# Kernel tuning notes

Hardware: AMD Instinct MI355X
Metric: run time of the kernel (lower is better)

## Reference

```python
import jax, jax.numpy as jnp
import numpy as np

DIM = 1024
HEADS = 16
HEAD_DIM = DIM // HEADS
SCALE = float(HEAD_DIM) ** -0.5


def setup_inputs() -> dict:
    key = jax.random.key(0)
    k1, k2, k3 = jax.random.split(key, 3)
    x = jax.random.normal(k1, (4, 2048, DIM), dtype=jnp.float32)
    w_qkv = jax.random.normal(k2, (DIM, 3 * DIM), dtype=jnp.float32) * (DIM ** -0.5)
    b_qkv = jnp.zeros((3 * DIM,), dtype=jnp.float32)
    w_proj = jax.random.normal(k3, (DIM, DIM), dtype=jnp.float32) * (DIM ** -0.5)
    b_proj = jnp.zeros((DIM,), dtype=jnp.float32)
    return {"x": x, "w_qkv": w_qkv, "b_qkv": b_qkv, "w_proj": w_proj, "b_proj": b_proj}


def reference(x, w_qkv, b_qkv, w_proj, b_proj):
    B, N, D = x.shape
    # QKV projection -> [B, N, 3, H, Dh] -> split
    qkv = (x @ w_qkv + b_qkv).reshape(B, N, 3, HEADS, HEAD_DIM)
    q = qkv[:, :, 0].transpose(0, 2, 1, 3)  # [B, H, N, Dh]
    k = qkv[:, :, 1].transpose(0, 2, 1, 3)
    v = qkv[:, :, 2].transpose(0, 2, 1, 3)
    att = jnp.einsum("bhnd,bhmd->bhnm", q, k) * SCALE  # [B, H, N, N]
    att = jax.nn.softmax(att, axis=-1)
    out = jnp.einsum("bhnm,bhmd->bhnd", att, v)  # [B, H, N, Dh]
    out = out.transpose(0, 2, 1, 3).reshape(B, N, D)
    return out @ w_proj + b_proj
```

## Files before the change

### kernel.cpp

```cpp
#include <hip/hip_runtime.h>


typedef __attribute__((ext_vector_type(8))) short bf8v;
typedef __attribute__((ext_vector_type(4))) short bf4v;
typedef __attribute__((ext_vector_type(4))) float f32x4;

#define DEVINL __device__ __forceinline__

DEVINL unsigned short f2bf(float x){
    unsigned int u = __float_as_uint(x);
    return (unsigned short)((u + 0x7FFFu + ((u >> 16) & 1u)) >> 16);
}
DEVINL float bf2f(unsigned short b){ return __uint_as_float(((unsigned int)b) << 16); }

union BV { bf8v v; unsigned int u[4]; };

DEVINL void gload16(const unsigned short* g, unsigned short* l){
    __builtin_amdgcn_global_load_lds(
        (const __attribute__((address_space(1))) unsigned int*)g,
        (__attribute__((address_space(3))) unsigned int*)l, 16, 0, 0);
}

__global__ __launch_bounds__(256) void split_rm(const float* __restrict__ in,
        unsigned short* __restrict__ oh, int n4){
    int i = blockIdx.x * 256 + threadIdx.x;
    if (i >= n4) return;
    float4 v = reinterpret_cast<const float4*>(in)[i];
    float vv[4] = {v.x, v.y, v.z, v.w};
    bf4v h;
#pragma unroll
    for (int j = 0; j < 4; ++j) h[j] = (short)f2bf(vv[j]);
    *reinterpret_cast<bf4v*>(oh + (size_t)i * 4) = h;
}

__global__ __launch_bounds__(256) void transpose_split(const float* __restrict__ in,
        unsigned short* __restrict__ oh,
        int K, int N){
    __shared__ float tile[32][33];
    int n0 = blockIdx.x * 32, k0 = blockIdx.y * 32;
    int c = threadIdx.x & 31, r0 = threadIdx.x >> 5;
#pragma unroll
    for (int j = 0; j < 4; ++j){
        int r = r0 + j * 8;
        tile[r][c] = in[(size_t)(k0 + r) * N + n0 + c];
    }
    __syncthreads();
#pragma unroll
    for (int j = 0; j < 4; ++j){
        int r = r0 + j * 8;
        float v = tile[c][r];
        oh[(size_t)(n0 + r) * K + k0 + c] = f2bf(v);
    }
}

template<int EPI, int NPL>
__global__ __launch_bounds__(256) void gemm3k(
    const unsigned short* __restrict__ Ah, const unsigned short* __restrict__ Al,
    const unsigned short* __restrict__ Bh,
    const float* __restrict__ bias, float* __restrict__ outf,
    unsigned short* __restrict__ Qh,
    unsigned short* __restrict__ Kh,
    unsigned short* __restrict__ Vth)
{
    __shared__ unsigned short AldsH[3][4096];
    __shared__ unsigned short AldsL[NPL == 2 ? 3 : 1][4096];
    __shared__ unsigned short Blds [3][4096];
    const int t = threadIdx.x;
    const int l = t & 63, g = l >> 4, wv = t >> 6;
    const int wr = wv >> 1, wc = wv & 1;
    const int bm = blockIdx.y * 128, bn = blockIdx.x * 128;
    const int srow = t >> 2;
    const int scol = ((t & 3) ^ ((t >> 3) & 3)) * 8;

    f32x4 acc[4][4] = {};

    auto stage = [&](int kt, int buf){
        int klocal = kt * 32;
#pragma unroll
        for (int j = 0; j < 2; ++j){
            size_t ro = (size_t)(bm + j*64 + srow) * 1024 + klocal + scol;
            gload16(Ah + ro, &AldsH[buf][j*2048 + wv*512]);
            if (NPL == 2) gload16(Al + ro, &AldsL[buf][j*2048 + wv*512]);
            gload16(Bh + (size_t)(bn + j*64 + srow) * 1024 + klocal + scol,
                    &Blds[buf][j*2048 + wv*512]);
        }
    };
    auto compute = [&](int cur){
        bf8v afh[4], bfv[4];
#pragma unroll
        for (int mf = 0; mf < 4; ++mf){
            int ar = wr*64 + mf*16 + (l & 15);
            afh[mf] = *reinterpret_cast<const bf8v*>(
                &AldsH[cur][ar*32 + (g ^ ((ar >> 1) & 3))*8]);
        }
#pragma unroll
        for (int nf = 0; nf < 4; ++nf){
            int br = wc*64 + nf*16 + (l & 15);
            bfv[nf] = *reinterpret_cast<const bf8v*>(
                &Blds[cur][br*32 + (g ^ ((br >> 1) & 3))*8]);
        }
#pragma unroll
        for (int mf = 0; mf < 4; ++mf)
#pragma unroll
            for (int nf = 0; nf < 4; ++nf)
                acc[mf][nf] = __builtin_amdgcn_mfma_f32_16x16x32_bf16(afh[mf], bfv[nf], acc[mf][nf], 0, 0, 0);
        if (NPL == 2){
            bf8v afl[4];
#pragma unroll
            for (int mf = 0; mf < 4; ++mf){
                int ar = wr*64 + mf*16 + (l & 15);
                afl[mf] = *reinterpret_cast<const bf8v*>(
                    &AldsL[NPL == 2 ? cur : 0][ar*32 + (g ^ ((ar >> 1) & 3))*8]);
            }
#pragma unroll
            for (int mf = 0; mf < 4; ++mf)
#pragma unroll
                for (int nf = 0; nf < 4; ++nf)
                    acc[mf][nf] = __builtin_amdgcn_mfma_f32_16x16x32_bf16(afl[mf], bfv[nf], acc[mf][nf], 0, 0, 0);
        }
    };

    stage(0, 0);
    stage(1, 1);
    if constexpr (NPL == 2) asm volatile("s_waitcnt vmcnt(6)" ::: "memory");
    else                    asm volatile("s_waitcnt vmcnt(4)" ::: "memory");
    __builtin_amdgcn_s_barrier();
    __builtin_amdgcn_sched_barrier(0);

    int cur = 0, nxt = 1, nx2 = 2;
#pragma unroll 1
    for (int kt = 0; kt < 32; ++kt){
        if (kt + 2 < 32) stage(kt + 2, nx2);
        compute(cur);
        if (kt + 1 < 32){
            if (kt + 2 < 32){
                if constexpr (NPL == 2) asm volatile("s_waitcnt vmcnt(6)" ::: "memory");
                else                    asm volatile("s_waitcnt vmcnt(4)" ::: "memory");
            } else {
                asm volatile("s_waitcnt vmcnt(0)" ::: "memory");
            }
            __builtin_amdgcn_s_barrier();
            __builtin_amdgcn_sched_barrier(0);
        }
        int tmp = cur; cur = nxt; nxt = nx2; nx2 = tmp;
    }
#pragma unroll
    for (int mf = 0; mf < 4; ++mf)
#pragma unroll
    for (int nf = 0; nf < 4; ++nf)
#pragma unroll
    for (int r = 0; r < 4; ++r){
        int n = bn + wc*64 + nf*16 + (l & 15);
        int m = bm + wr*64 + mf*16 + g*4 + r;
        float v = acc[mf][nf][r] + bias[n];
        if (EPI == 0){
            int sec = n >> 10;
            int nn = n & 1023, hh = nn >> 6, dh = nn & 63;
            int bb = m >> 11, tok = m & 2047;
            if (sec == 0) v *= 0.18033688011112042f;
            unsigned short hb = f2bf(v);
            if (sec == 2){
                int tok2 = (tok & ~31) | (((tok >> 2) & 3) << 3) | (tok & 3) | (((tok >> 4) & 1) << 2);
                tok2 = (tok2 & ~31) | ((tok2 & 31) ^ (((dh >> 1) & 3) << 3));
                size_t o = ((size_t)((bb*16 + hh)*64 + dh)) * 2048 + tok2;
                Vth[o] = hb;
            } else if (sec == 1){
                size_t o = ((size_t)((bb*16 + hh)*2048 + tok)) * 64 + (dh ^ ((tok & 7) << 3));
                Kh[o] = hb;
            } else {
                size_t o = ((size_t)((bb*16 + hh)*2048 + tok)) * 64 + dh;
                Qh[o] = hb;
            }
        } else {
            outf[(size_t)m * 1024 + n] = v;
        }
    }
}

__global__ __launch_bounds__(256, 4) void attn(
    const unsigned short* __restrict__ Qh,
    const unsigned short* __restrict__ Kh,
    const unsigned short* __restrict__ Vth,
    unsigned short* __restrict__ Oh, unsigned short* __restrict__ Ol)
{
    __shared__ unsigned short Klds[3][2048];
    __shared__ unsigned short Vlds[3][2048];
    const int t = threadIdx.x, l = t & 63, g = l >> 4, wv = t >> 6;
    const int bid = (int)((blockIdx.x & 7) * 128 + (blockIdx.x >> 3));
    const int qt = bid & 15, hh = (bid >> 4) & 15, bb = bid >> 8;
    const int bh = bb * 16 + hh;
    const int q0 = qt * 128 + wv * 32;

    const unsigned short* Kbh = Kh  + (size_t)bh * 131072;
    const unsigned short* Vbh = Vth + (size_t)bh * 131072;

    const int kst = (t >> 3) * 64   + (t & 7) * 8;
    const int vst = (t >> 2) * 2048 + (t & 3) * 8;

    bf8v qh_[2][2];
#pragma unroll
    for (int nf = 0; nf < 2; ++nf){
        size_t ro = ((size_t)bh * 2048 + q0 + nf*16 + (l & 15)) * 64 + g * 8;
#pragma unroll
        for (int ks = 0; ks < 2; ++ks)
            qh_[nf][ks] = *reinterpret_cast<const bf8v*>(Qh + ro + ks*32);
    }
    f32x4 ot[4][2] = {};
    float l_run[2] = {0.f, 0.f};

    auto stage = [&](int it, int buf){
        gload16(Kbh + it*2048 + kst, &Klds[buf][wv*512]);
        gload16(Vbh + it*32   + vst, &Vlds[buf][wv*512]);
    };
    auto step = [&](int cur){
        bf8v kf[2][2], vf[4];
#pragma unroll
        for (int mf = 0; mf < 2; ++mf){
            int r = (l & 15) + 16*mf;
#pragma unroll
            for (int ks = 0; ks < 2; ++ks)
                kf[mf][ks] = *reinterpret_cast<const bf8v*>(
                    &Klds[cur][r*64 + ((g*8 + ks*32) ^ ((r & 7) << 3))]);
        }
#pragma unroll
        for (int mf = 0; mf < 4; ++mf){
            int dh = (l & 15) + 16*mf;
            vf[mf] = *reinterpret_cast<const bf8v*>(
                &Vlds[cur][dh*32 + ((g*8) ^ (((dh >> 1) & 3) << 3))]);
        }
        f32x4 s[2][2] = {};
        __builtin_amdgcn_s_setprio(1);
#pragma unroll
        for (int mf = 0; mf < 2; ++mf)
#pragma unroll
        for (int nf = 0; nf < 2; ++nf)
#pragma unroll
        for (int ks = 0; ks < 2; ++ks)
            s[mf][nf] = __builtin_amdgcn_mfma_f32_16x16x32_bf16(kf[mf][ks], qh_[nf][ks], s[mf][nf], 0,0,0);
        __builtin_amdgcn_s_setprio(0);
        BV ph[2];
#pragma unroll
        for (int nf = 0; nf < 2; ++nf){
            float p[8];
#pragma unroll
            for (int mf = 0; mf < 2; ++mf)
#pragma unroll
            for (int r = 0; r < 4; ++r)
                p[mf*4 + r] = __builtin_amdgcn_exp2f(s[mf][nf][r]);
            l_run[nf] += ((p[0]+p[1]) + (p[2]+p[3])) + ((p[4]+p[5]) + (p[6]+p[7]));
#pragma unroll
            for (int i = 0; i < 4; ++i)
                asm("v_cvt_pk_bf16_f32 %0, %1, %2"
                    : "=v"(ph[nf].u[i]) : "v"(p[2*i]), "v"(p[2*i+1]));
        }
        __builtin_amdgcn_s_setprio(1);
#pragma unroll
        for (int mf = 0; mf < 4; ++mf)
#pragma unroll
        for (int nf = 0; nf < 2; ++nf)
            ot[mf][nf] = __builtin_amdgcn_mfma_f32_16x16x32_bf16(vf[mf], ph[nf].v, ot[mf][nf], 0,0,0);
        __builtin_amdgcn_s_setprio(0);
    };

    stage(0, 0);
    stage(1, 1);
    asm volatile("s_waitcnt vmcnt(2)" ::: "memory");
    __builtin_amdgcn_s_barrier();
    __builtin_amdgcn_sched_barrier(0);

    int cur = 0, nxt = 1, nx2 = 2;
#pragma unroll 1
    for (int it = 0; it < 64; ++it){
        if (it + 2 < 64) stage(it + 2, nx2);
        step(cur);
        if (it + 1 < 64){
            if (it + 2 < 64) asm volatile("s_waitcnt vmcnt(2)" ::: "memory");
            else             asm volatile("s_waitcnt vmcnt(0)" ::: "memory");
            __builtin_amdgcn_s_barrier();
            __builtin_amdgcn_sched_barrier(0);
        }
        int tmp = cur; cur = nxt; nxt = nx2; nx2 = tmp;
    }
#pragma unroll
    for (int nf = 0; nf < 2; ++nf){
        float lr = l_run[nf];
        lr += __shfl_xor(lr, 16);
        lr += __shfl_xor(lr, 32);
        float inv = 1.f / lr;
        int tok = q0 + nf*16 + (l & 15);
#pragma unroll
        for (int mf = 0; mf < 4; ++mf){
            bf4v hv, lv;
#pragma unroll
            for (int r = 0; r < 4; ++r){
                float v = ot[mf][nf][r] * inv;
                unsigned short hb = f2bf(v);
                hv[r] = (short)hb;
                lv[r] = (short)f2bf(v - bf2f(hb));
            }
            size_t o = ((size_t)(bb * 2048 + tok)) * 1024 + hh*64 + mf*16 + g*4;
            *reinterpret_cast<bf4v*>(Oh + o) = hv;
            *reinterpret_cast<bf4v*>(Ol + o) = lv;
        }
    }
}

extern "C" void kernel_launch(void* const* d_in, const int* in_sizes, int n_in,
                              void* d_out, int out_size, void* d_ws, size_t ws_size,
                              hipStream_t stream) {
    (void)in_sizes; (void)n_in; (void)out_size; (void)ws_size;
    const float* x      = (const float*)d_in[0];
    const float* w_qkv  = (const float*)d_in[1];
    const float* b_qkv  = (const float*)d_in[2];
    const float* w_proj = (const float*)d_in[3];
    const float* b_proj = (const float*)d_in[4];
    float* out = (float*)d_out;

    char* w = (char*)d_ws;
    unsigned short* XH  = (unsigned short*)(w + 0);
    unsigned short* ATL = (unsigned short*)(w + 16777216);
    unsigned short* QH  = (unsigned short*)(w + 33554432);
    unsigned short* KH  = (unsigned short*)(w + 67108864);
    unsigned short* VTH = (unsigned short*)(w + 100663296);
    unsigned short* WQH = (unsigned short*)(w + 134217728);
    unsigned short* WPH = (unsigned short*)(w + 140509184);
    unsigned short* ATH = XH;

    split_rm<<<8192, 256, 0, stream>>>(x, XH, 2097152);
    transpose_split<<<dim3(96, 32), 256, 0, stream>>>(w_qkv, WQH, 1024, 3072);
    transpose_split<<<dim3(32, 32), 256, 0, stream>>>(w_proj, WPH, 1024, 1024);
    gemm3k<0,1><<<dim3(24, 64), 256, 0, stream>>>(XH, nullptr, WQH, b_qkv, nullptr,
                                                  QH, KH, VTH);
    attn<<<1024, 256, 0, stream>>>(QH, KH, VTH, ATH, ATL);
    gemm3k<1,2><<<dim3(8, 64), 256, 0, stream>>>(ATH, ATL, WPH, b_proj, out,
                                                 nullptr, nullptr, nullptr);
}
```

Baseline: 223.3 us.

## Process two 32-key chunks per pipeline stage in attention loop

Each iteration of the attention main loop now stages and computes 64 keys (two 32-key chunks) instead of 32, halving the iteration count and the number of barriers and waitcnt sync points. The LDS K/V ring buffers double in size and launch bounds drop from 4 to 3 blocks per SM to fit the larger footprint and register use. The cost is lower occupancy and more live score registers per wave, which could offset the savings in synchronisation overhead.

```diff
diff --git a/kernel.cpp b/kernel.cpp
--- a/kernel.cpp
+++ b/kernel.cpp
@@ -177,14 +177,14 @@
     }
 }
 
-__global__ __launch_bounds__(256, 4) void attn(
+__global__ __launch_bounds__(256, 3) void attn(
     const unsigned short* __restrict__ Qh,
     const unsigned short* __restrict__ Kh,
     const unsigned short* __restrict__ Vth,
     unsigned short* __restrict__ Oh, unsigned short* __restrict__ Ol)
 {
-    __shared__ unsigned short Klds[3][2048];
-    __shared__ unsigned short Vlds[3][2048];
+    __shared__ unsigned short Klds[3][4096];
+    __shared__ unsigned short Vlds[3][4096];
     const int t = threadIdx.x, l = t & 63, g = l >> 4, wv = t >> 6;
     const int bid = (int)((blockIdx.x & 7) * 128 + (blockIdx.x >> 3));
     const int qt = bid & 15, hh = (bid >> 4) & 15, bb = bid >> 8;
@@ -209,72 +209,86 @@
     float l_run[2] = {0.f, 0.f};
 
     auto stage = [&](int it, int buf){
-        gload16(Kbh + it*2048 + kst, &Klds[buf][wv*512]);
-        gload16(Vbh + it*32   + vst, &Vlds[buf][wv*512]);
+#pragma unroll
+        for (int kc = 0; kc < 2; ++kc){
+            int it2 = it * 2 + kc;
+            gload16(Kbh + it2*2048 + kst, &Klds[buf][kc*2048 + wv*512]);
+            gload16(Vbh + it2*32   + vst, &Vlds[buf][kc*2048 + wv*512]);
+        }
     };
     auto step = [&](int cur){
-        bf8v kf[2][2], vf[4];
-#pragma unroll
-        for (int mf = 0; mf < 2; ++mf){
-            int r = (l & 15) + 16*mf;
+        f32x4 s[4][2] = {};
+#pragma unroll
+        for (int kc = 0; kc < 2; ++kc){
+            bf8v kf[2][2];
+#pragma unroll
+            for (int mt = 0; mt < 2; ++mt){
+                int r = (l & 15) + 16*mt;
+#pragma unroll
+                for (int ks = 0; ks < 2; ++ks)
+                    kf[mt][ks] = *reinterpret_cast<const bf8v*>(
+                        &Klds[cur][kc*2048 + r*64 + ((g*8 + ks*32) ^ ((r & 7) << 3))]);
+            }
+            __builtin_amdgcn_s_setprio(1);
+#pragma unroll
+            for (int mt = 0; mt < 2; ++mt)
+#pragma unroll
+            for (int nf = 0; nf < 2; ++nf)
 #pragma unroll
             for (int ks = 0; ks < 2; ++ks)
-                kf[mf][ks] = *reinterpret_cast<const bf8v*>(
-                    &Klds[cur][r*64 + ((g*8 + ks*32) ^ ((r & 7) << 3))]);
+                s[kc*2+mt][nf] = __builtin_amdgcn_mfma_f32_16x16x32_bf16(kf[mt][ks], qh_[nf][ks], s[kc*2+mt][nf], 0,0,0);
+            __builtin_amdgcn_s_setprio(0);
+        }
+        BV ph[2][2];
+#pragma unroll
+        for (int nf = 0; nf < 2; ++nf){
+            float p[16];
+#pragma unroll
+            for (int kt = 0; kt < 4; ++kt)
+#pragma unroll
+            for (int r = 0; r < 4; ++r)
+                p[kt*4 + r] = __builtin_amdgcn_exp2f(s[kt][nf][r]);
+            float s0 = ((p[0]+p[1]) + (p[2]+p[3])) + ((p[4]+p[5]) + (p[6]+p[7]));
+            float s1 = ((p[8]+p[9]) + (p[10]+p[11])) + ((p[12]+p[13]) + (p[14]+p[15]));
+            l_run[nf] += s0 + s1;
+#pragma unroll
+            for (int kc = 0; kc < 2; ++kc)
+#pragma unroll
+            for (int i = 0; i < 4; ++i)
+                asm("v_cvt_pk_bf16_f32 %0, %1, %2"
+                    : "=v"(ph[nf][kc].u[i]) : "v"(p[kc*8 + 2*i]), "v"(p[kc*8 + 2*i + 1]));
         }
 #pragma unroll
         for (int mf = 0; mf < 4; ++mf){
             int dh = (l & 15) + 16*mf;
-            vf[mf] = *reinterpret_cast<const bf8v*>(
-                &Vlds[cur][dh*32 + ((g*8) ^ (((dh >> 1) & 3) << 3))]);
-        }
-        f32x4 s[2][2] = {};
-        __builtin_amdgcn_s_setprio(1);
-#pragma unroll
-        for (int mf = 0; mf < 2; ++mf)
-#pragma unroll
-        for (int nf = 0; nf < 2; ++nf)
-#pragma unroll
-        for (int ks = 0; ks < 2; ++ks)
-            s[mf][nf] = __builtin_amdgcn_mfma_f32_16x16x32_bf16(kf[mf][ks], qh_[nf][ks], s[mf][nf], 0,0,0);
-        __builtin_amdgcn_s_setprio(0);
-        BV ph[2];
-#pragma unroll
-        for (int nf = 0; nf < 2; ++nf){
-            float p[8];
-#pragma unroll
-            for (int mf = 0; mf < 2; ++mf)
-#pragma unroll
-            for (int r = 0; r < 4; ++r)
-                p[mf*4 + r] = __builtin_amdgcn_exp2f(s[mf][nf][r]);
-            l_run[nf] += ((p[0]+p[1]) + (p[2]+p[3])) + ((p[4]+p[5]) + (p[6]+p[7]));
-#pragma unroll
-            for (int i = 0; i < 4; ++i)
-                asm("v_cvt_pk_bf16_f32 %0, %1, %2"
-                    : "=v"(ph[nf].u[i]) : "v"(p[2*i]), "v"(p[2*i+1]));
-        }
-        __builtin_amdgcn_s_setprio(1);
-#pragma unroll
-        for (int mf = 0; mf < 4; ++mf)
-#pragma unroll
-        for (int nf = 0; nf < 2; ++nf)
-            ot[mf][nf] = __builtin_amdgcn_mfma_f32_16x16x32_bf16(vf[mf], ph[nf].v, ot[mf][nf], 0,0,0);
-        __builtin_amdgcn_s_setprio(0);
+            bf8v vf[2];
+#pragma unroll
+            for (int kc = 0; kc < 2; ++kc)
+                vf[kc] = *reinterpret_cast<const bf8v*>(
+                    &Vlds[cur][kc*2048 + dh*32 + ((g*8) ^ (((dh >> 1) & 3) << 3))]);
+            __builtin_amdgcn_s_setprio(1);
+#pragma unroll
+            for (int nf = 0; nf < 2; ++nf)
+#pragma unroll
+            for (int kc = 0; kc < 2; ++kc)
+                ot[mf][nf] = __builtin_amdgcn_mfma_f32_16x16x32_bf16(vf[kc], ph[nf][kc].v, ot[mf][nf], 0,0,0);
+            __builtin_amdgcn_s_setprio(0);
+        }
     };
 
     stage(0, 0);
     stage(1, 1);
-    asm volatile("s_waitcnt vmcnt(2)" ::: "memory");
+    asm volatile("s_waitcnt vmcnt(4)" ::: "memory");
     __builtin_amdgcn_s_barrier();
     __builtin_amdgcn_sched_barrier(0);
 
     int cur = 0, nxt = 1, nx2 = 2;
 #pragma unroll 1
-    for (int it = 0; it < 64; ++it){
-        if (it + 2 < 64) stage(it + 2, nx2);
+    for (int it = 0; it < 32; ++it){
+        if (it + 2 < 32) stage(it + 2, nx2);
         step(cur);
-        if (it + 1 < 64){
-            if (it + 2 < 64) asm volatile("s_waitcnt vmcnt(2)" ::: "memory");
+        if (it + 1 < 32){
+            if (it + 2 < 32) asm volatile("s_waitcnt vmcnt(4)" ::: "memory");
             else             asm volatile("s_waitcnt vmcnt(0)" ::: "memory");
             __builtin_amdgcn_s_barrier();
             __builtin_amdgcn_sched_barrier(0);
```

Result: slower. 228.9 us (+2.5%).

## Use 256x256 tiles with 8 waves for QKV GEMM; split projection kernel

Applied to the files above, without the earlier changes.

The QKV projection GEMM moves from 128x128 tiles with 4 waves to 256x256 tiles with 8 waves (each wave computes 128x64). This doubles operand reuse per LDS load and halves global traffic per output. The grid shrinks to 384 blocks, which may not fill all CUs evenly, and per-thread accumulator registers double. The projection GEMM is split into its own non-templated kernel whose hi and lo A fragments are loaded together, plus some refactoring of the scatter epilogue.

```diff
diff --git a/kernel.cpp b/kernel.cpp
--- a/kernel.cpp
+++ b/kernel.cpp
@@ -19,6 +19,29 @@
     __builtin_amdgcn_global_load_lds(
         (const __attribute__((address_space(1))) unsigned int*)g,
         (__attribute__((address_space(3))) unsigned int*)l, 16, 0, 0);
+}
+
+DEVINL void qkv_scatter(int m, int n, float v,
+    unsigned short* __restrict__ Qh, unsigned short* __restrict__ Kh,
+    unsigned short* __restrict__ Vth)
+{
+    int sec = n >> 10;
+    int nn = n & 1023, hh = nn >> 6, dh = nn & 63;
+    int bb = m >> 11, tok = m & 2047;
+    if (sec == 0) v *= 0.18033688011112042f;
+    unsigned short hb = f2bf(v);
+    if (sec == 2){
+        int tok2 = (tok & ~31) | (((tok >> 2) & 3) << 3) | (tok & 3) | (((tok >> 4) & 1) << 2);
+        tok2 = (tok2 & ~31) | ((tok2 & 31) ^ (((dh >> 1) & 3) << 3));
+        size_t o = ((size_t)((bb*16 + hh)*64 + dh)) * 2048 + tok2;
+        Vth[o] = hb;
+    } else if (sec == 1){
+        size_t o = ((size_t)((bb*16 + hh)*2048 + tok)) * 64 + (dh ^ ((tok & 7) << 3));
+        Kh[o] = hb;
+    } else {
+        size_t o = ((size_t)((bb*16 + hh)*2048 + tok)) * 64 + dh;
+        Qh[o] = hb;
+    }
 }
 
 __global__ __launch_bounds__(256) void split_rm(const float* __restrict__ in,
@@ -53,17 +76,94 @@
     }
 }
 
-template<int EPI, int NPL>
-__global__ __launch_bounds__(256) void gemm3k(
-    const unsigned short* __restrict__ Ah, const unsigned short* __restrict__ Al,
+__global__ __launch_bounds__(512) void gemm256(
+    const unsigned short* __restrict__ Ah,
     const unsigned short* __restrict__ Bh,
-    const float* __restrict__ bias, float* __restrict__ outf,
+    const float* __restrict__ bias,
     unsigned short* __restrict__ Qh,
     unsigned short* __restrict__ Kh,
     unsigned short* __restrict__ Vth)
 {
+    __shared__ unsigned short Alds[3][8192];
+    __shared__ unsigned short Blds[3][8192];
+    const int t = threadIdx.x;
+    const int l = t & 63, g = l >> 4, wid = t >> 6;
+    const int wr = wid >> 2, wc = wid & 3;
+    const int bm = blockIdx.y * 256, bn = blockIdx.x * 256;
+    const int srow = t >> 2;
+    const int scol = ((t & 3) ^ ((t >> 3) & 3)) * 8;
+
+    f32x4 acc[8][4] = {};
+
+    auto stage = [&](int kt, int buf){
+        int klocal = kt * 32;
+#pragma unroll
+        for (int j = 0; j < 2; ++j){
+            gload16(Ah + (size_t)(bm + j*128 + srow) * 1024 + klocal + scol,
+                    &Alds[buf][j*4096 + wid*512]);
+            gload16(Bh + (size_t)(bn + j*128 + srow) * 1024 + klocal + scol,
+                    &Blds[buf][j*4096 + wid*512]);
+        }
+    };
+    auto compute = [&](int cur){
+        bf8v af[8], bfv[4];
+#pragma unroll
+        for (int mf = 0; mf < 8; ++mf){
+            int ar = wr*128 + mf*16 + (l & 15);
+            af[mf] = *reinterpret_cast<const bf8v*>(
+                &Alds[cur][ar*32 + (g ^ ((ar >> 1) & 3))*8]);
+        }
+#pragma unroll
+        for (int nf = 0; nf < 4; ++nf){
+            int br = wc*64 + nf*16 + (l & 15);
+            bfv[nf] = *reinterpret_cast<const bf8v*>(
+                &Blds[cur][br*32 + (g ^ ((br >> 1) & 3))*8]);
+        }
+#pragma unroll
+        for (int mf = 0; mf < 8; ++mf)
+#pragma unroll
+            for (int nf = 0; nf < 4; ++nf)
+                acc[mf][nf] = __builtin_amdgcn_mfma_f32_16x16x32_bf16(af[mf], bfv[nf], acc[mf][nf], 0, 0, 0);
+    };
+
+    stage(0, 0);
+    stage(1, 1);
+    asm volatile("s_waitcnt vmcnt(4)" ::: "memory");
+    __builtin_amdgcn_s_barrier();
+    __builtin_amdgcn_sched_barrier(0);
+
+    int cur = 0, nxt = 1, nx2 = 2;
+#pragma unroll 1
+    for (int kt = 0; kt < 32; ++kt){
+        if (kt + 2 < 32) stage(kt + 2, nx2);
+        compute(cur);
+        if (kt + 1 < 32){
+            if (kt + 2 < 32) asm volatile("s_waitcnt vmcnt(4)" ::: "memory");
+            else             asm volatile("s_waitcnt vmcnt(0)" ::: "memory");
+            __builtin_amdgcn_s_barrier();
+            __builtin_amdgcn_sched_barrier(0);
+        }
+        int tmp = cur; cur = nxt; nxt = nx2; nx2 = tmp;
+    }
+#pragma unroll
+    for (int mf = 0; mf < 8; ++mf)
+#pragma unroll
+    for (int nf = 0; nf < 4; ++nf)
+#pragma unroll
+    for (int r = 0; r < 4; ++r){
+        int n = bn + wc*64 + nf*16 + (l & 15);
+        int m = bm + wr*128 + mf*16 + g*4 + r;
+        qkv_scatter(m, n, acc[mf][nf][r] + bias[n], Qh, Kh, Vth);
+    }
+}
+
+__global__ __launch_bounds__(256) void gemm_proj(
+    const unsigned short* __restrict__ Ah, const unsigned short* __restrict__ Al,
+    const unsigned short* __restrict__ Bh,
+    const float* __restrict__ bias, float* __restrict__ outf)
+{
     __shared__ unsigned short AldsH[3][4096];
-    __shared__ unsigned short AldsL[NPL == 2 ? 3 : 1][4096];
+    __shared__ unsigned short AldsL[3][4096];
     __shared__ unsigned short Blds [3][4096];
     const int t = threadIdx.x;
     const int l = t & 63, g = l >> 4, wv = t >> 6;
@@ -80,18 +180,19 @@
         for (int j = 0; j < 2; ++j){
             size_t ro = (size_t)(bm + j*64 + srow) * 1024 + klocal + scol;
             gload16(Ah + ro, &AldsH[buf][j*2048 + wv*512]);
-            if (NPL == 2) gload16(Al + ro, &AldsL[buf][j*2048 + wv*512]);
+            gload16(Al + ro, &AldsL[buf][j*2048 + wv*512]);
             gload16(Bh + (size_t)(bn + j*64 + srow) * 1024 + klocal + scol,
                     &Blds[buf][j*2048 + wv*512]);
         }
     };
     auto compute = [&](int cur){
-        bf8v afh[4], bfv[4];
+        bf8v afh[4], afl[4], bfv[4];
 #pragma unroll
         for (int mf = 0; mf < 4; ++mf){
             int ar = wr*64 + mf*16 + (l & 15);
-            afh[mf] = *reinterpret_cast<const bf8v*>(
-                &AldsH[cur][ar*32 + (g ^ ((ar >> 1) & 3))*8]);
+            int ao = ar*32 + (g ^ ((ar >> 1) & 3))*8;
+            afh[mf] = *reinterpret_cast<const bf8v*>(&AldsH[cur][ao]);
+            afl[mf] = *reinterpret_cast<const bf8v*>(&AldsL[cur][ao]);
         }
 #pragma unroll
         for (int nf = 0; nf < 4; ++nf){
@@ -104,26 +205,16 @@
 #pragma unroll
             for (int nf = 0; nf < 4; ++nf)
                 acc[mf][nf] = __builtin_amdgcn_mfma_f32_16x16x32_bf16(afh[mf], bfv[nf], acc[mf][nf], 0, 0, 0);
-        if (NPL == 2){
-            bf8v afl[4];
-#pragma unroll
-            for (int mf = 0; mf < 4; ++mf){
-                int ar = wr*64 + mf*16 + (l & 15);
-                afl[mf] = *reinterpret_cast<const bf8v*>(
-                    &AldsL[NPL == 2 ? cur : 0][ar*32 + (g ^ ((ar >> 1) & 3))*8]);
-            }
-#pragma unroll
-            for (int mf = 0; mf < 4; ++mf)
-#pragma unroll
-                for (int nf = 0; nf < 4; ++nf)
-                    acc[mf][nf] = __builtin_amdgcn_mfma_f32_16x16x32_bf16(afl[mf], bfv[nf], acc[mf][nf], 0, 0, 0);
-        }
+#pragma unroll
+        for (int mf = 0; mf < 4; ++mf)
+#pragma unroll
+            for (int nf = 0; nf < 4; ++nf)
+                acc[mf][nf] = __builtin_amdgcn_mfma_f32_16x16x32_bf16(afl[mf], bfv[nf], acc[mf][nf], 0, 0, 0);
     };
 
     stage(0, 0);
     stage(1, 1);
-    if constexpr (NPL == 2) asm volatile("s_waitcnt vmcnt(6)" ::: "memory");
-    else                    asm volatile("s_waitcnt vmcnt(4)" ::: "memory");
+    asm volatile("s_waitcnt vmcnt(6)" ::: "memory");
     __builtin_amdgcn_s_barrier();
     __builtin_amdgcn_sched_barrier(0);
 
@@ -133,12 +224,8 @@
         if (kt + 2 < 32) stage(kt + 2, nx2);
         compute(cur);
         if (kt + 1 < 32){
-            if (kt + 2 < 32){
-                if constexpr (NPL == 2) asm volatile("s_waitcnt vmcnt(6)" ::: "memory");
-                else                    asm volatile("s_waitcnt vmcnt(4)" ::: "memory");
-            } else {
-                asm volatile("s_waitcnt vmcnt(0)" ::: "memory");
-            }
+            if (kt + 2 < 32) asm volatile("s_waitcnt vmcnt(6)" ::: "memory");
+            else             asm volatile("s_waitcnt vmcnt(0)" ::: "memory");
             __builtin_amdgcn_s_barrier();
             __builtin_amdgcn_sched_barrier(0);
         }
@@ -152,28 +239,7 @@
     for (int r = 0; r < 4; ++r){
         int n = bn + wc*64 + nf*16 + (l & 15);
         int m = bm + wr*64 + mf*16 + g*4 + r;
-        float v = acc[mf][nf][r] + bias[n];
-        if (EPI == 0){
-            int sec = n >> 10;
-            int nn = n & 1023, hh = nn >> 6, dh = nn & 63;
-            int bb = m >> 11, tok = m & 2047;
-            if (sec == 0) v *= 0.18033688011112042f;
-            unsigned short hb = f2bf(v);
-            if (sec == 2){
-                int tok2 = (tok & ~31) | (((tok >> 2) & 3) << 3) | (tok & 3) | (((tok >> 4) & 1) << 2);
-                tok2 = (tok2 & ~31) | ((tok2 & 31) ^ (((dh >> 1) & 3) << 3));
-                size_t o = ((size_t)((bb*16 + hh)*64 + dh)) * 2048 + tok2;
-                Vth[o] = hb;
-            } else if (sec == 1){
-                size_t o = ((size_t)((bb*16 + hh)*2048 + tok)) * 64 + (dh ^ ((tok & 7) << 3));
-                Kh[o] = hb;
-            } else {
-                size_t o = ((size_t)((bb*16 + hh)*2048 + tok)) * 64 + dh;
-                Qh[o] = hb;
-            }
-        } else {
-            outf[(size_t)m * 1024 + n] = v;
-        }
+        outf[(size_t)m * 1024 + n] = acc[mf][nf][r] + bias[n];
     }
 }
 
@@ -329,9 +395,7 @@
     split_rm<<<8192, 256, 0, stream>>>(x, XH, 2097152);
     transpose_split<<<dim3(96, 32), 256, 0, stream>>>(w_qkv, WQH, 1024, 3072);
     transpose_split<<<dim3(32, 32), 256, 0, stream>>>(w_proj, WPH, 1024, 1024);
-    gemm3k<0,1><<<dim3(24, 64), 256, 0, stream>>>(XH, nullptr, WQH, b_qkv, nullptr,
-                                                  QH, KH, VTH);
+    gemm256<<<dim3(12, 32), 512, 0, stream>>>(XH, WQH, b_qkv, QH, KH, VTH);
     attn<<<1024, 256, 0, stream>>>(QH, KH, VTH, ATH, ATL);
-    gemm3k<1,2><<<dim3(8, 64), 256, 0, stream>>>(ATH, ATL, WPH, b_proj, out,
-                                                 nullptr, nullptr, nullptr);
-}
+    gemm_proj<<<dim3(8, 64), 256, 0, stream>>>(ATH, ATL, WPH, b_proj, out);
+}
```

Result: slower. 250.5 us, median of 2 (+12.2%).
